# Kernel optimization log

Hardware: AMD Instinct MI355X
Metric: run time of the kernel (lower is better)

Reference implementation:

```python
import jax, jax.numpy as jnp
import numpy as np

N = 30000   # nodes
E = 480000  # edges
C = 64      # in_channels
NC = 101    # num_classes
K1 = 5      # kernel_size per dim
K = K1 * K1 # 25 kernel weight matrices (dim=2)


def _spline_conv(x, src, dst, pseudo, W, root, bias):
    """SplineConv, degree-1 open B-spline, dim=2, kernel_size=5, aggr='mean'.
    x: [N,C_in], pseudo: [E,2] in [0,1], W: [25,C_in,C_out], root: [C_in,C_out].
    """
    n, c = x.shape
    v = pseudo * (K1 - 1)                       # [E,2] in [0, K1-1]
    bot = jnp.clip(jnp.floor(v), 0, K1 - 1)
    frac = v - bot                              # fractional part
    bot_i = bot.astype(jnp.int32)
    bits = jnp.array([[0, 0], [0, 1], [1, 0], [1, 1]], dtype=jnp.int32)  # S=4 combos
    idx_d = jnp.clip(bot_i[:, None, :] + bits[None, :, :], 0, K1 - 1)    # [E,4,2]
    w_d = jnp.where(bits[None, :, :] == 1, frac[:, None, :], 1.0 - frac[:, None, :])
    B = w_d[..., 0] * w_d[..., 1]               # [E,4] basis weights
    kidx = idx_d[..., 0] * K1 + idx_d[..., 1]   # [E,4] flat kernel index in [0,25)
    msg = B[:, :, None] * x[src][:, None, :]    # [E,4,C] weighted source feats
    seg = (dst[:, None] * K + kidx).reshape(-1) # combined (node,kernel) segment id
    acc = jax.ops.segment_sum(msg.reshape(-1, c), seg, num_segments=n * K)
    acc = acc.reshape(n, K, c)                  # [N,25,C]
    out = jnp.einsum('nkc,kcd->nd', acc, W)     # apply kernel weight matrices
    deg = jax.ops.segment_sum(jnp.ones(dst.shape[0], x.dtype), dst, num_segments=n)
    out = out / jnp.maximum(deg, 1.0)[:, None]  # mean aggregation
    out = out + x @ root                        # root weight
    if bias is not None:
        out = out + bias
    return out


def _bn(x, g, b):
    m = x.mean(0)
    v = x.var(0)
    return g * (x - m) * jax.lax.rsqrt(v + 1e-5) + b


def setup_inputs() -> dict:
    key = jax.random.key(0)
    ks = jax.random.split(key, 30)
    p = lambda k, shape: jax.random.normal(k, shape, jnp.float32) * 0.05
    d = {
        'x': jax.random.normal(ks[0], (N, C), jnp.float32),
        'edge_attr': jax.random.uniform(ks[1], (E, 3), dtype=jnp.float32),
        'src': jax.random.randint(ks[2], (E,), 0, N),
        'dst': jax.random.randint(ks[3], (E,), 0, N),
    }
    for i, name in enumerate(['conv1', 'conv2', 'conv3']):
        d[name + '_W'] = p(ks[4 + 2 * i], (K, C, C))
        d[name + '_root'] = p(ks[5 + 2 * i], (C, C))
        d['norm%d_gamma' % (i + 1)] = jnp.ones((C,), jnp.float32)
        d['norm%d_beta' % (i + 1)] = jnp.zeros((C,), jnp.float32)
    for j, (name, oc) in enumerate([('regr', 4), ('cls', NC), ('obj', 1)]):
        d[name + '_W'] = p(ks[10 + 3 * j], (K, C, oc))
        d[name + '_root'] = p(ks[11 + 3 * j], (C, oc))
        d[name + '_bias'] = jnp.zeros((oc,), jnp.float32)
    return d


def reference(x, edge_attr, src, dst,
              conv1_W, conv1_root, norm1_gamma, norm1_beta,
              conv2_W, conv2_root, norm2_gamma, norm2_beta,
              conv3_W, conv3_root, norm3_gamma, norm3_beta,
              regr_W, regr_root, regr_bias,
              cls_W, cls_root, cls_bias,
              obj_W, obj_root, obj_bias):
    pseudo = edge_attr[:, :2]
    x1 = jax.nn.relu(_bn(_spline_conv(x, src, dst, pseudo, conv1_W, conv1_root, None), norm1_gamma, norm1_beta))
    x2 = jax.nn.relu(_bn(_spline_conv(x1, src, dst, pseudo, conv2_W, conv2_root, None), norm2_gamma, norm2_beta))
    x3 = jax.nn.relu(_bn(_spline_conv(x1, src, dst, pseudo, conv3_W, conv3_root, None), norm3_gamma, norm3_beta))
    reg = _spline_conv(x2, src, dst, pseudo, regr_W, regr_root, regr_bias)
    cls = _spline_conv(x3, src, dst, pseudo, cls_W, cls_root, cls_bias)
    obj = _spline_conv(x3, src, dst, pseudo, obj_W, obj_root, obj_bias)
    return (cls, reg, obj)
```

## Files before the change

### kernel.cpp

```cpp
#include <hip/hip_runtime.h>
#include <hip/hip_bf16.h>

#define NN 30000
#define NE 480000
#define CIN 64
#define KD 1600
#define KT 1664
#define KMAC 13
#define BM 64
#define NBLK 469
#define MROWS (NBLK*BM)
#define REG_OFF  (30000*101)
#define OBJ_OFF  (30000*105)

typedef short bf16x8 __attribute__((ext_vector_type(8)));
typedef float f32x4  __attribute__((ext_vector_type(4)));

__device__ __forceinline__ ushort f2bf(float x) {
    union { float f; unsigned u; } v; v.f = x;
    unsigned r = v.u + 0x7FFFu + ((v.u >> 16) & 1u);
    return (ushort)(r >> 16);
}

__global__ void k_count(const int* __restrict__ dst, int* __restrict__ deg) {
    int e = blockIdx.x * 256 + threadIdx.x;
    if (e < NE) atomicAdd(&deg[dst[e]], 1);
}

__global__ void k_scan(const int* __restrict__ deg, int* __restrict__ rp,
                       int* __restrict__ cur, float* __restrict__ invd) {
    __shared__ int s[1024];
    int t = threadIdx.x;
    const int CH = 30;
    int base = t * CH, loc = 0;
    for (int i = 0; i < CH; ++i) { int n = base + i; if (n < NN) loc += deg[n]; }
    s[t] = loc; __syncthreads();
    for (int o = 1; o < 1024; o <<= 1) {
        int v = (t >= o) ? s[t - o] : 0;
        __syncthreads(); s[t] += v; __syncthreads();
    }
    int run = s[t] - loc;
    for (int i = 0; i < CH; ++i) {
        int n = base + i;
        if (n < NN) {
            int dg = deg[n];
            rp[n] = run; cur[n] = run;
            invd[n] = 1.f / (float)(dg > 0 ? dg : 1);
            run += dg;
        }
    }
    if (t == 0) rp[NN] = NE;
}

__global__ void k_scatter(const float* __restrict__ ea, const int* __restrict__ src,
                          const int* __restrict__ dst, int* __restrict__ cur,
                          float4* __restrict__ mB, int2* __restrict__ mI) {
    int e = blockIdx.x * 256 + threadIdx.x;
    if (e >= NE) return;
    float p0 = ea[e*3+0], p1 = ea[e*3+1];
    float v0 = p0*4.f, v1 = p1*4.f;
    float b0 = fminf(fmaxf(floorf(v0),0.f),4.f);
    float b1 = fminf(fmaxf(floorf(v1),0.f),4.f);
    float f0 = v0-b0, f1 = v1-b1;
    int i0 = (int)b0, i1 = (int)b1;
    float B00 = (1.f-f0)*(1.f-f1);
    float B01 = (1.f-f0)*f1;
    float B10 = f0*(1.f-f1);
    float B11 = f0*f1;
    int k00 = i0*5 + i1;
    int dn = dst[e];
    int pos = atomicAdd(&cur[dn], 1);
    mB[pos] = make_float4(B00,B01,B10,B11);
    mI[pos] = make_int2(k00, src[e]);
}

__global__ void k_prepw(const float* W1,const float* R1,const float* W2,const float* R2,
                        const float* W3,const float* R3,const float* Wr,const float* Rr,
                        const float* Wc,const float* Rc,const float* Wo,const float* Ro,
                        ushort* T1, ushort* T23, ushort* Tr, ushort* TcTo) {
    int b = blockIdx.x;
    const float* W; const float* R; ushort* T; int od; int col;
    if      (b < 64)  { W=W1; R=R1; T=T1  + (long)b*KT;       od=64;  col=b;     }
    else if (b < 128) { W=W2; R=R2; T=T23 + (long)(b-64)*KT;  od=64;  col=b-64;  }
    else if (b < 192) { W=W3; R=R3; T=T23 + (long)(b-64)*KT;  od=64;  col=b-128; }
    else if (b < 208) { W=Wr; R=Rr; T=Tr  + (long)(b-192)*KT; od=4;   col=b-192; }
    else if (b < 320) { W=Wc; R=Rc; T=TcTo+ (long)(b-208)*KT; od=101; col=b-208; }
    else              { W=Wo; R=Ro; T=TcTo+ (long)(b-208)*KT; od=1;   col=b-320; }
    for (int kc = threadIdx.x; kc < KT; kc += 256) {
        float v = 0.f;
        if (col < od) v = (kc < KD) ? W[(long)kc*od + col] : R[(long)(kc-KD)*od + col];
        T[kc] = f2bf(v);
    }
}

#define AGGC(K, A_, B_, C_, D_) case K: A_ += bb.x*xu; B_ += bb.y*xu; C_ += bb.z*xu; D_ += bb.w*xu; break;

template<bool NORM>
__global__ void k_agg(const int* __restrict__ rp, const float4* __restrict__ mB,
                      const int2* __restrict__ mI, const float* __restrict__ f,
                      const float* __restrict__ invd,
                      const float* __restrict__ st, const float* __restrict__ g,
                      const float* __restrict__ be, ushort* __restrict__ A) {
    int wid = (blockIdx.x * 256 + threadIdx.x) >> 6;
    wid = __builtin_amdgcn_readfirstlane(wid);
    int l = threadIdx.x & 63;
    if (wid >= NN) return;
    float na = 0.f, nc = 0.f;
    if (NORM) {
        const float inv_n = 1.f / (float)NN;
        float mm = st[l] * inv_n;
        float var = st[64 + l] * inv_n - mm * mm;
        float rs = rsqrtf(var + 1e-5f);
        na = g[l] * rs; nc = be[l] - mm * na;
    }
    float a00=0.f,a01=0.f,a02=0.f,a03=0.f,a04=0.f;
    float a05=0.f,a06=0.f,a07=0.f,a08=0.f,a09=0.f;
    float a10=0.f,a11=0.f,a12=0.f,a13=0.f,a14=0.f;
    float a15=0.f,a16=0.f,a17=0.f,a18=0.f,a19=0.f;
    float a20=0.f,a21=0.f,a22=0.f,a23=0.f,a24=0.f;
    int beg = rp[wid], end = rp[wid + 1];
    for (int e0 = beg; e0 < end; e0 += 8) {
        int2 m[8];
        #pragma unroll
        for (int u = 0; u < 8; ++u) {
            int e = e0 + u;
            m[u] = mI[(e < end) ? e : beg];
        }
        float xv[8];
        #pragma unroll
        for (int u = 0; u < 8; ++u) xv[u] = f[(long)m[u].y * CIN + l];
        __builtin_amdgcn_sched_barrier(0);
        float4 b[8];
        #pragma unroll
        for (int u = 0; u < 8; ++u) {
            int e = e0 + u;
            b[u] = mB[(e < end) ? e : beg];
            if (e >= end) b[u] = make_float4(0,0,0,0);
        }
        __builtin_amdgcn_sched_barrier(0);
        #pragma unroll
        for (int u = 0; u < 8; ++u) {
            float xu = xv[u];
            if (NORM) xu = fmaxf(xu * na + nc, 0.f);
            int k00 = __builtin_amdgcn_readfirstlane(m[u].x);
            float4 bb = b[u];
            switch (k00) {
                AGGC(0,  a00,a01,a05,a06)
                AGGC(1,  a01,a02,a06,a07)
                AGGC(2,  a02,a03,a07,a08)
                AGGC(3,  a03,a04,a08,a09)
                AGGC(5,  a05,a06,a10,a11)
                AGGC(6,  a06,a07,a11,a12)
                AGGC(7,  a07,a08,a12,a13)
                AGGC(8,  a08,a09,a13,a14)
                AGGC(10, a10,a11,a15,a16)
                AGGC(11, a11,a12,a16,a17)
                AGGC(12, a12,a13,a17,a18)
                AGGC(13, a13,a14,a18,a19)
                AGGC(15, a15,a16,a20,a21)
                AGGC(16, a16,a17,a21,a22)
                AGGC(17, a17,a18,a22,a23)
                AGGC(18, a18,a19,a23,a24)
                default: break;
            }
        }
    }
    float s = invd[wid];
    ushort* rb = A + (long)wid * KT + l;
    #define STO(K, V) rb[K*CIN] = f2bf((V) * s);
    STO(0,a00)  STO(1,a01)  STO(2,a02)  STO(3,a03)  STO(4,a04)
    STO(5,a05)  STO(6,a06)  STO(7,a07)  STO(8,a08)  STO(9,a09)
    STO(10,a10) STO(11,a11) STO(12,a12) STO(13,a13) STO(14,a14)
    STO(15,a15) STO(16,a16) STO(17,a17) STO(18,a18) STO(19,a19)
    STO(20,a20) STO(21,a21) STO(22,a22) STO(23,a23) STO(24,a24)
    #undef STO
    float rv = f[(long)wid * CIN + l];
    if (NORM) rv = fmaxf(rv * na + nc, 0.f);
    rb[KD] = f2bf(rv);
}

template<int MODE>
__global__ void k_gemm(const ushort* __restrict__ A, const ushort* __restrict__ B,
                       float* __restrict__ o0, float* __restrict__ o1,
                       float* __restrict__ s0, float* __restrict__ s1,
                       const float* __restrict__ b0, const float* __restrict__ b1) {
    __shared__ ushort As[2 * 8192];
    f32x4* part = (f32x4*)As;
    const int tid = threadIdx.x, w = tid >> 6, l = tid & 63;
    const int m0 = blockIdx.x * BM;

    int colrow;
    if constexpr (MODE == 0)      colrow = ((w & 3) << 4) + (l & 15);
    else if constexpr (MODE == 2) colrow = (l & 15);
    else                          colrow = (w << 4) + (l & 15);
    const ushort* Bp = B + (long)colrow * KT + ((l >> 4) << 3);

    const int r0 = tid >> 4, j0 = tid & 15;
    const ushort* Asrc0 = A + (long)(m0 + r0) * KT + (j0 << 3);
    const ushort* Asrc1 = A + (long)(m0 + 32 + r0) * KT + (j0 << 3);
    const int swzo = ((j0 ^ (r0 & 7)) << 4);

    f32x4 acc[4];
    #pragma unroll
    for (int m = 0; m < 4; ++m) acc[m] = (f32x4){0.f,0.f,0.f,0.f};

    {
        int4 v0 = *(const int4*)(Asrc0);
        int4 v1 = *(const int4*)(Asrc1);
        char* basep = (char*)As;
        *(int4*)(basep + r0 * 256 + swzo) = v0;
        *(int4*)(basep + (32 + r0) * 256 + swzo) = v1;
    }
    __syncthreads();

    int buf = 0;
    for (int ks = 0; ks < KMAC; ++ks) {
        int4 v0, v1;
        if (ks < KMAC - 1) {
            v0 = *(const int4*)(Asrc0 + (ks + 1) * 128);
            v1 = *(const int4*)(Asrc1 + (ks + 1) * 128);
        }
        bool act;
        if constexpr (MODE == 0)      act = (w < 4) ? (ks < 7) : (ks >= 7);
        else if constexpr (MODE == 2) act = ((ks & 7) == w);
        else                          act = true;
        if (act) {
            const char* Ab = (const char*)As + buf * 16384;
            #pragma unroll
            for (int s = 0; s < 4; ++s) {
                bf16x8 bb = *(const bf16x8*)(Bp + ks * 128 + s * 32);
                #pragma unroll
                for (int m = 0; m < 4; ++m) {
                    int r = (m << 4) + (l & 15);
                    int j = (s << 2) + (l >> 4);
                    bf16x8 a = *(const bf16x8*)(Ab + r * 256 + ((j ^ (r & 7)) << 4));
                    acc[m] = __builtin_amdgcn_mfma_f32_16x16x32_bf16(a, bb, acc[m], 0, 0, 0);
                }
            }
        }
        if (ks < KMAC - 1) {
            char* basep = (char*)As + (buf ^ 1) * 16384;
            *(int4*)(basep + r0 * 256 + swzo) = v0;
            *(int4*)(basep + (32 + r0) * 256 + swzo) = v1;
        }
        __syncthreads();
        buf ^= 1;
    }

    auto emit = [&](f32x4* ac, float* out, int ostride, int col, int odcap, float bv, float* stats) {
        float p1 = 0.f, p2 = 0.f;
        #pragma unroll
        for (int m = 0; m < 4; ++m) {
            #pragma unroll
            for (int r = 0; r < 4; ++r) {
                int row = m0 + (m << 4) + ((l >> 4) << 2) + r;
                if (row < NN) {
                    float v = ac[m][r] + bv;
                    if (col < odcap) out[(long)row * ostride + col] = v;
                    p1 += v; p2 += v * v;
                }
            }
        }
        if (stats) {
            p1 += __shfl_down(p1, 32); p2 += __shfl_down(p2, 32);
            p1 += __shfl_down(p1, 16); p2 += __shfl_down(p2, 16);
            if (l < 16) { atomicAdd(&stats[col], p1); atomicAdd(&stats[64 + col], p2); }
        }
    };

    if constexpr (MODE == 0) {
        if (w >= 4) {
            #pragma unroll
            for (int m = 0; m < 4; ++m) part[((w & 3) << 8) + (l << 2) + m] = acc[m];
        }
        __syncthreads();
        if (w < 4) {
            #pragma unroll
            for (int m = 0; m < 4; ++m) acc[m] += part[((w & 3) << 8) + (l << 2) + m];
            emit(acc, o0, 64, ((w & 3) << 4) + (l & 15), 64, 0.f, s0);
        }
    } else if constexpr (MODE == 1) {
        if (w < 4) emit(acc, o0, 64, (w << 4) + (l & 15), 64, 0.f, s0);
        else       emit(acc, o1, 64, ((w - 4) << 4) + (l & 15), 64, 0.f, s1);
    } else if constexpr (MODE == 2) {
        if (w > 0) {
            #pragma unroll
            for (int m = 0; m < 4; ++m) part[((w - 1) << 8) + (l << 2) + m] = acc[m];
        }
        __syncthreads();
        if (w == 0) {
            for (int i = 0; i < 7; ++i) {
                #pragma unroll
                for (int m = 0; m < 4; ++m) acc[m] += part[(i << 8) + (l << 2) + m];
            }
            int col = l & 15;
            emit(acc, o0, 4, col, 4, (col < 4) ? b0[col] : 0.f, nullptr);
        }
    } else {
        if (w < 7) {
            int col = (w << 4) + (l & 15);
            emit(acc, o0, 101, col, 101, (col < 101) ? b0[col] : 0.f, nullptr);
        } else {
            int col = l & 15;
            emit(acc, o1, 1, col, 1, b1[0], nullptr);
        }
    }
}

extern "C" void kernel_launch(void* const* d_in, const int* in_sizes, int n_in,
                              void* d_out, int out_size, void* d_ws, size_t ws_size,
                              hipStream_t stream) {
    const float* x    = (const float*)d_in[0];
    const float* ea   = (const float*)d_in[1];
    const int*   src  = (const int*)d_in[2];
    const int*   dst  = (const int*)d_in[3];
    const float* W1   = (const float*)d_in[4];
    const float* R1   = (const float*)d_in[5];
    const float* g1   = (const float*)d_in[6];
    const float* be1  = (const float*)d_in[7];
    const float* W2   = (const float*)d_in[8];
    const float* R2   = (const float*)d_in[9];
    const float* g2   = (const float*)d_in[10];
    const float* be2  = (const float*)d_in[11];
    const float* W3   = (const float*)d_in[12];
    const float* R3   = (const float*)d_in[13];
    const float* g3   = (const float*)d_in[14];
    const float* be3  = (const float*)d_in[15];
    const float* Wr   = (const float*)d_in[16];
    const float* Rr   = (const float*)d_in[17];
    const float* br   = (const float*)d_in[18];
    const float* Wc   = (const float*)d_in[19];
    const float* Rc   = (const float*)d_in[20];
    const float* bc   = (const float*)d_in[21];
    const float* Wo   = (const float*)d_in[22];
    const float* Ro   = (const float*)d_in[23];
    const float* bo   = (const float*)d_in[24];
    float* out = (float*)d_out;

    char* p = (char*)d_ws;
    auto alloc = [&](size_t bytes) { char* r = p; p += (bytes + 255) & ~(size_t)255; return r; };
    float4* mB   = (float4*)alloc((size_t)NE * 16);
    int2*   mI   = (int2*)  alloc((size_t)NE * 8);
    int*    deg  = (int*)   alloc((size_t)NN * 4);
    int*    rp   = (int*)   alloc((size_t)(NN + 1) * 4);
    int*    cur  = (int*)   alloc((size_t)NN * 4);
    float*  invd = (float*) alloc((size_t)NN * 4);
    ushort* T1   = (ushort*)alloc((size_t)64  * KT * 2);
    ushort* T23  = (ushort*)alloc((size_t)128 * KT * 2);
    ushort* Tr   = (ushort*)alloc((size_t)16  * KT * 2);
    ushort* TcTo = (ushort*)alloc((size_t)128 * KT * 2);
    float*  y1   = (float*) alloc((size_t)NN * CIN * 4);
    float*  y2   = (float*) alloc((size_t)NN * CIN * 4);
    float*  y3   = (float*) alloc((size_t)NN * CIN * 4);
    float*  stats= (float*) alloc(3 * 128 * 4);
    ushort* A    = (ushort*)alloc((size_t)MROWS * KT * 2);
    float* st1 = stats, *st2 = stats + 128, *st3 = stats + 256;

    hipMemsetAsync(deg, 0, (size_t)NN * 4, stream);
    hipMemsetAsync(stats, 0, 3 * 128 * 4, stream);

    k_count  <<<1875, 256, 0, stream>>>(dst, deg);
    k_scan   <<<1, 1024, 0, stream>>>(deg, rp, cur, invd);
    k_scatter<<<1875, 256, 0, stream>>>(ea, src, dst, cur, mB, mI);
    k_prepw  <<<336, 256, 0, stream>>>(W1,R1,W2,R2,W3,R3,Wr,Rr,Wc,Rc,Wo,Ro,T1,T23,Tr,TcTo);

    k_agg<false><<<7500, 256, 0, stream>>>(rp, mB, mI, x, invd, nullptr, nullptr, nullptr, A);
    k_gemm<0><<<NBLK, 512, 0, stream>>>(A, T1, y1, nullptr, st1, nullptr, nullptr, nullptr);
    k_agg<true><<<7500, 256, 0, stream>>>(rp, mB, mI, y1, invd, st1, g1, be1, A);
    k_gemm<1><<<NBLK, 512, 0, stream>>>(A, T23, y2, y3, st2, st3, nullptr, nullptr);
    k_agg<true><<<7500, 256, 0, stream>>>(rp, mB, mI, y2, invd, st2, g2, be2, A);
    k_gemm<2><<<NBLK, 512, 0, stream>>>(A, Tr, out + REG_OFF, nullptr, nullptr, nullptr, br, nullptr);
    k_agg<true><<<7500, 256, 0, stream>>>(rp, mB, mI, y3, invd, st3, g3, be3, A);
    k_gemm<3><<<NBLK, 512, 0, stream>>>(A, TcTo, out, out + OBJ_OFF, nullptr, nullptr, bc, bo);
}
```

Measured before the change: 465.1 us.

## Halve GEMM row tile and replace single-block scan with three-pass multi-block scan

The GEMM row tile shrinks from 64 to 32 rows, doubling the block count to 938. Each block loads a single A row per thread and keeps two MFMA accumulators instead of four, so per-block LDS use halves and occupancy and CU coverage improve. The one-block 1024-thread degree prefix scan becomes three kernels: per-block reduce, a scan of the block sums, and a per-block scan with offsets. This removes a serial single-block bottleneck but adds two extra launches, and each B-fragment load is now reused across only two row tiles instead of four.

New measurement: 450.2 us. 3.2% less time.

```diff
diff --git a/kernel.cpp b/kernel.cpp
--- a/kernel.cpp
+++ b/kernel.cpp
@@ -7,9 +7,10 @@
 #define KD 1600
 #define KT 1664
 #define KMAC 13
-#define BM 64
-#define NBLK 469
+#define BM 32
+#define NBLK 938
 #define MROWS (NBLK*BM)
+#define NBS 118
 #define REG_OFF  (30000*101)
 #define OBJ_OFF  (30000*105)
 
@@ -27,29 +28,47 @@
     if (e < NE) atomicAdd(&deg[dst[e]], 1);
 }
 
-__global__ void k_scan(const int* __restrict__ deg, int* __restrict__ rp,
-                       int* __restrict__ cur, float* __restrict__ invd) {
-    __shared__ int s[1024];
+__global__ void k_scan1(const int* __restrict__ deg, int* __restrict__ bsum) {
+    __shared__ int sred[4];
+    int i = blockIdx.x * 256 + threadIdx.x;
+    int v = (i < NN) ? deg[i] : 0;
+    #pragma unroll
+    for (int o = 32; o >= 1; o >>= 1) v += __shfl_down(v, o);
+    int w = threadIdx.x >> 6, l = threadIdx.x & 63;
+    if (l == 0) sred[w] = v;
+    __syncthreads();
+    if (threadIdx.x == 0) bsum[blockIdx.x] = sred[0] + sred[1] + sred[2] + sred[3];
+}
+
+__global__ void k_scan2(const int* __restrict__ bsum, int* __restrict__ boff) {
+    __shared__ int s[128];
     int t = threadIdx.x;
-    const int CH = 30;
-    int base = t * CH, loc = 0;
-    for (int i = 0; i < CH; ++i) { int n = base + i; if (n < NN) loc += deg[n]; }
-    s[t] = loc; __syncthreads();
-    for (int o = 1; o < 1024; o <<= 1) {
-        int v = (t >= o) ? s[t - o] : 0;
-        __syncthreads(); s[t] += v; __syncthreads();
-    }
-    int run = s[t] - loc;
-    for (int i = 0; i < CH; ++i) {
-        int n = base + i;
-        if (n < NN) {
-            int dg = deg[n];
-            rp[n] = run; cur[n] = run;
-            invd[n] = 1.f / (float)(dg > 0 ? dg : 1);
-            run += dg;
-        }
-    }
-    if (t == 0) rp[NN] = NE;
+    int v = (t < NBS) ? bsum[t] : 0;
+    s[t] = v; __syncthreads();
+    for (int o = 1; o < 128; o <<= 1) {
+        int u = (t >= o) ? s[t - o] : 0;
+        __syncthreads(); s[t] += u; __syncthreads();
+    }
+    if (t < NBS) boff[t] = s[t] - v;
+}
+
+__global__ void k_scan3(const int* __restrict__ deg, const int* __restrict__ boff,
+                        int* __restrict__ rp, int* __restrict__ cur, float* __restrict__ invd) {
+    __shared__ int s[256];
+    int t = threadIdx.x;
+    int i = blockIdx.x * 256 + t;
+    int v = (i < NN) ? deg[i] : 0;
+    s[t] = v; __syncthreads();
+    for (int o = 1; o < 256; o <<= 1) {
+        int u = (t >= o) ? s[t - o] : 0;
+        __syncthreads(); s[t] += u; __syncthreads();
+    }
+    int ex = s[t] - v + boff[blockIdx.x];
+    if (i < NN) {
+        rp[i] = ex; cur[i] = ex;
+        invd[i] = 1.f / (float)(v > 0 ? v : 1);
+    }
+    if (i == NN - 1) rp[NN] = NE;
 }
 
 __global__ void k_scatter(const float* __restrict__ ea, const int* __restrict__ src,
@@ -184,7 +203,7 @@
                        float* __restrict__ o0, float* __restrict__ o1,
                        float* __restrict__ s0, float* __restrict__ s1,
                        const float* __restrict__ b0, const float* __restrict__ b1) {
-    __shared__ ushort As[2 * 8192];
+    __shared__ ushort As[2 * 4096];
     f32x4* part = (f32x4*)As;
     const int tid = threadIdx.x, w = tid >> 6, l = tid & 63;
     const int m0 = blockIdx.x * BM;
@@ -196,41 +215,31 @@
     const ushort* Bp = B + (long)colrow * KT + ((l >> 4) << 3);
 
     const int r0 = tid >> 4, j0 = tid & 15;
-    const ushort* Asrc0 = A + (long)(m0 + r0) * KT + (j0 << 3);
-    const ushort* Asrc1 = A + (long)(m0 + 32 + r0) * KT + (j0 << 3);
+    const ushort* Asrc = A + (long)(m0 + r0) * KT + (j0 << 3);
     const int swzo = ((j0 ^ (r0 & 7)) << 4);
 
-    f32x4 acc[4];
-    #pragma unroll
-    for (int m = 0; m < 4; ++m) acc[m] = (f32x4){0.f,0.f,0.f,0.f};
-
-    {
-        int4 v0 = *(const int4*)(Asrc0);
-        int4 v1 = *(const int4*)(Asrc1);
-        char* basep = (char*)As;
-        *(int4*)(basep + r0 * 256 + swzo) = v0;
-        *(int4*)(basep + (32 + r0) * 256 + swzo) = v1;
-    }
+    f32x4 acc[2];
+    acc[0] = (f32x4){0.f,0.f,0.f,0.f};
+    acc[1] = (f32x4){0.f,0.f,0.f,0.f};
+
+    *(int4*)((char*)As + r0 * 256 + swzo) = *(const int4*)(Asrc);
     __syncthreads();
 
     int buf = 0;
     for (int ks = 0; ks < KMAC; ++ks) {
-        int4 v0, v1;
-        if (ks < KMAC - 1) {
-            v0 = *(const int4*)(Asrc0 + (ks + 1) * 128);
-            v1 = *(const int4*)(Asrc1 + (ks + 1) * 128);
-        }
+        int4 vn;
+        if (ks < KMAC - 1) vn = *(const int4*)(Asrc + (ks + 1) * 128);
         bool act;
         if constexpr (MODE == 0)      act = (w < 4) ? (ks < 7) : (ks >= 7);
         else if constexpr (MODE == 2) act = ((ks & 7) == w);
         else                          act = true;
         if (act) {
-            const char* Ab = (const char*)As + buf * 16384;
+            const char* Ab = (const char*)As + buf * 8192;
             #pragma unroll
             for (int s = 0; s < 4; ++s) {
                 bf16x8 bb = *(const bf16x8*)(Bp + ks * 128 + s * 32);
                 #pragma unroll
-                for (int m = 0; m < 4; ++m) {
+                for (int m = 0; m < 2; ++m) {
                     int r = (m << 4) + (l & 15);
                     int j = (s << 2) + (l >> 4);
                     bf16x8 a = *(const bf16x8*)(Ab + r * 256 + ((j ^ (r & 7)) << 4));
@@ -238,11 +247,8 @@
                 }
             }
         }
-        if (ks < KMAC - 1) {
-            char* basep = (char*)As + (buf ^ 1) * 16384;
-            *(int4*)(basep + r0 * 256 + swzo) = v0;
-            *(int4*)(basep + (32 + r0) * 256 + swzo) = v1;
-        }
+        if (ks < KMAC - 1)
+            *(int4*)((char*)As + (buf ^ 1) * 8192 + r0 * 256 + swzo) = vn;
         __syncthreads();
         buf ^= 1;
     }
@@ -250,7 +256,7 @@
     auto emit = [&](f32x4* ac, float* out, int ostride, int col, int odcap, float bv, float* stats) {
         float p1 = 0.f, p2 = 0.f;
         #pragma unroll
-        for (int m = 0; m < 4; ++m) {
+        for (int m = 0; m < 2; ++m) {
             #pragma unroll
             for (int r = 0; r < 4; ++r) {
                 int row = m0 + (m << 4) + ((l >> 4) << 2) + r;
@@ -271,12 +277,12 @@
     if constexpr (MODE == 0) {
         if (w >= 4) {
             #pragma unroll
-            for (int m = 0; m < 4; ++m) part[((w & 3) << 8) + (l << 2) + m] = acc[m];
+            for (int m = 0; m < 2; ++m) part[((w & 3) << 7) + (l << 1) + m] = acc[m];
         }
         __syncthreads();
         if (w < 4) {
             #pragma unroll
-            for (int m = 0; m < 4; ++m) acc[m] += part[((w & 3) << 8) + (l << 2) + m];
+            for (int m = 0; m < 2; ++m) acc[m] += part[((w & 3) << 7) + (l << 1) + m];
             emit(acc, o0, 64, ((w & 3) << 4) + (l & 15), 64, 0.f, s0);
         }
     } else if constexpr (MODE == 1) {
@@ -285,13 +291,13 @@
     } else if constexpr (MODE == 2) {
         if (w > 0) {
             #pragma unroll
-            for (int m = 0; m < 4; ++m) part[((w - 1) << 8) + (l << 2) + m] = acc[m];
+            for (int m = 0; m < 2; ++m) part[((w - 1) << 7) + (l << 1) + m] = acc[m];
         }
         __syncthreads();
         if (w == 0) {
             for (int i = 0; i < 7; ++i) {
                 #pragma unroll
-                for (int m = 0; m < 4; ++m) acc[m] += part[(i << 8) + (l << 2) + m];
+                for (int m = 0; m < 2; ++m) acc[m] += part[(i << 7) + (l << 1) + m];
             }
             int col = l & 15;
             emit(acc, o0, 4, col, 4, (col < 4) ? b0[col] : 0.f, nullptr);
@@ -345,6 +351,8 @@
     int*    rp   = (int*)   alloc((size_t)(NN + 1) * 4);
     int*    cur  = (int*)   alloc((size_t)NN * 4);
     float*  invd = (float*) alloc((size_t)NN * 4);
+    int*    bsum = (int*)   alloc((size_t)NBS * 4);
+    int*    boff = (int*)   alloc((size_t)NBS * 4);
     ushort* T1   = (ushort*)alloc((size_t)64  * KT * 2);
     ushort* T23  = (ushort*)alloc((size_t)128 * KT * 2);
     ushort* Tr   = (ushort*)alloc((size_t)16  * KT * 2);
@@ -360,7 +368,9 @@
     hipMemsetAsync(stats, 0, 3 * 128 * 4, stream);
 
     k_count  <<<1875, 256, 0, stream>>>(dst, deg);
-    k_scan   <<<1, 1024, 0, stream>>>(deg, rp, cur, invd);
+    k_scan1  <<<NBS, 256, 0, stream>>>(deg, bsum);
+    k_scan2  <<<1, 128, 0, stream>>>(bsum, boff);
+    k_scan3  <<<NBS, 256, 0, stream>>>(deg, boff, rp, cur, invd);
     k_scatter<<<1875, 256, 0, stream>>>(ea, src, dst, cur, mB, mI);
     k_prepw  <<<336, 256, 0, stream>>>(W1,R1,W2,R2,W3,R3,Wr,Rr,Wc,Rc,Wo,Ro,T1,T23,Tr,TcTo);
 
```
